# Kernel tuning notes

Measured on AMD Instinct MI355X. Metric: run time of the kernel, lower is better.

Reference implementation:

```python
import jax, jax.numpy as jnp
import numpy as np

F = 15          # features
H = 128         # hidden_features
L = 12          # num_layers
NB = 16         # num_bins
M = 3 * NB - 1  # 47 params per feature (tails='linear')
TAIL = 3.0
MIN_W = 1e-3; MIN_H = 1e-3; MIN_D = 1e-3
B = 65536


def _masks():
    # nflows MADE sequential degrees
    deg_in = np.arange(1, F + 1)                       # input degrees 1..F
    deg_h = np.arange(H) % (F - 1) + 1                 # hidden degrees
    m_init = (deg_h[:, None] >= deg_in[None, :]).astype(np.float32)  # [H,F]
    m_h = (deg_h[:, None] >= deg_h[None, :]).astype(np.float32)      # [H,H]
    deg_out = np.repeat(deg_in, M)                     # tile -> repeat_interleave, [F*M]
    m_out = (deg_out[:, None] > deg_h[None, :]).astype(np.float32)   # [F*M,H], strict for output
    return jnp.asarray(m_init), jnp.asarray(m_h), jnp.asarray(m_out)


def setup_inputs() -> dict:
    key = jax.random.key(0)
    ks = jax.random.split(key, 7)
    s = 0.05
    return {
        "x": jax.random.normal(ks[0], (B, F), jnp.float32),
        "W_init": jax.random.normal(ks[1], (L, H, F), jnp.float32) * s,
        "b_init": jax.random.normal(ks[2], (L, H), jnp.float32) * s,
        "W_res": jax.random.normal(ks[3], (L, 2, 2, H, H), jnp.float32) * s,
        "b_res": jax.random.normal(ks[4], (L, 2, 2, H), jnp.float32) * s,
        "W_out": jax.random.normal(ks[5], (L, F * M, H), jnp.float32) * s,
        "b_out": jax.random.normal(ks[6], (L, F * M), jnp.float32) * s,
    }


def _made(x, p, m_init, m_h, m_out):
    # MADE with 2 masked residual blocks (relu, no BN/dropout), as in nflows
    h = x @ (p["W_init"] * m_init).T + p["b_init"]
    for blk in range(2):
        t = jax.nn.relu(h)
        t = t @ (p["W_res"][blk, 0] * m_h).T + p["b_res"][blk, 0]
        t = jax.nn.relu(t)
        t = t @ (p["W_res"][blk, 1] * m_h).T + p["b_res"][blk, 1]
        h = h + t
    return h @ (p["W_out"] * m_out).T + p["b_out"]  # [B, F*M]


def _rqs_forward(x, params):
    # unconstrained rational-quadratic spline, tails='linear' (nflows)
    uw = params[..., :NB]
    uh = params[..., NB:2 * NB]
    ud = params[..., 2 * NB:]                          # [B,F,NB-1]
    const = float(np.log(np.exp(1.0 - MIN_D) - 1.0))
    ud = jnp.pad(ud, ((0, 0), (0, 0), (1, 1)), constant_values=const)  # [B,F,NB+1]

    inside = (x >= -TAIL) & (x <= TAIL)
    xc = jnp.clip(x, -TAIL, TAIL)

    w = jax.nn.softmax(uw, axis=-1)
    w = MIN_W + (1.0 - MIN_W * NB) * w
    cw = jnp.pad(jnp.cumsum(w, axis=-1), ((0, 0), (0, 0), (1, 0)))
    cw = 2.0 * TAIL * cw - TAIL
    cw = cw.at[..., 0].set(-TAIL).at[..., -1].set(TAIL)
    w = cw[..., 1:] - cw[..., :-1]

    hgt = jax.nn.softmax(uh, axis=-1)
    hgt = MIN_H + (1.0 - MIN_H * NB) * hgt
    ch = jnp.pad(jnp.cumsum(hgt, axis=-1), ((0, 0), (0, 0), (1, 0)))
    ch = 2.0 * TAIL * ch - TAIL
    ch = ch.at[..., 0].set(-TAIL).at[..., -1].set(TAIL)
    hgt = ch[..., 1:] - ch[..., :-1]

    d = MIN_D + jax.nn.softplus(ud)                    # [B,F,NB+1]

    idx = jnp.clip(jnp.sum((xc[..., None] >= cw).astype(jnp.int32), axis=-1) - 1, 0, NB - 1)[..., None]
    g = lambda a: jnp.take_along_axis(a, idx, axis=-1)[..., 0]

    in_cw, in_w, in_ch, in_h = g(cw), g(w), g(ch), g(hgt)
    in_delta = g(hgt / w)
    in_d, in_d1 = g(d), g(d[..., 1:])

    theta = (xc - in_cw) / in_w
    tomt = theta * (1.0 - theta)
    num = in_h * (in_delta * theta ** 2 + in_d * tomt)
    den = in_delta + (in_d + in_d1 - 2.0 * in_delta) * tomt
    y = in_ch + num / den
    dnum = in_delta ** 2 * (in_d1 * theta ** 2 + 2.0 * in_delta * tomt + in_d * (1.0 - theta) ** 2)
    lad = jnp.log(dnum) - 2.0 * jnp.log(den)

    y = jnp.where(inside, y, x)                        # identity tails
    lad = jnp.where(inside, lad, 0.0)
    return y, jnp.sum(lad, axis=-1)


def reference(x, W_init, b_init, W_res, b_res, W_out, b_out):
    m_init, m_h, m_out = _masks()
    params = {"W_init": W_init, "b_init": b_init, "W_res": W_res,
              "b_res": b_res, "W_out": W_out, "b_out": b_out}

    def step(carry, p):
        xx, ld = carry
        xx = xx[:, ::-1]                               # ReversePermutation
        raw = _made(xx, p, m_init, m_h, m_out)
        xx, lad = _rqs_forward(xx, raw.reshape(xx.shape[0], F, M))
        return (xx, ld + lad), None

    (z, logdet), _ = jax.lax.scan(step, (x, jnp.zeros(x.shape[0], x.dtype)), params)
    return z, logdet
```

## Files before the change

### kernel.cpp

```cpp
#include <hip/hip_runtime.h>
#include <hip/hip_bf16.h>

#define FDIM 15
#define HDIM 128
#define LNUM 12
#define NBINS 16
#define MDIM 47
#define FM 705
#define BATCH 65536
#define TAILF 3.0f
#define MIN_Wc 0.001f
#define MIN_Hc 0.001f
#define MIN_Dc 0.001f

typedef __bf16 bf16_t;
typedef __attribute__((ext_vector_type(8))) __bf16 bf16x8;
typedef __attribute__((ext_vector_type(4))) __bf16 bf16x4;
typedef __attribute__((ext_vector_type(4))) float f32x4;

#define FRAGS_USED 211
#define FRAGS_PAD 224
#define FRAG_ELEMS 512
#define RING 16
#define WFRAG_TOTAL (LNUM * FRAGS_PAD * FRAG_ELEMS)

#define BB_FLOATS 1360
#define BB_TOTAL (LNUM * BB_FLOATS)

#define SPW 32

__device__ __forceinline__ int perm_pos(int pos) {
    int r, o;
    if (pos < 20) { r = pos / 10; o = pos % 10; }
    else          { r = 2 + (pos - 20) / 9; o = (pos - 20) % 9; }
    return r + 14 * o;
}

__device__ __forceinline__ float sp_softplus(float u) {
    return (u > 20.f) ? u : __logf(1.f + __expf(u));
}

__global__ void preproc_kernel(const float* __restrict__ Wi,
                               const float* __restrict__ Wr,
                               const float* __restrict__ Wo,
                               const float* __restrict__ bIg,
                               const float* __restrict__ bRg,
                               const float* __restrict__ bOg,
                               bf16_t* __restrict__ wfrag,
                               float* __restrict__ bblob) {
    const int RES_OFF[8] = {0, 1, 3, 5, 8, 11, 15, 19};
    const int OUT_OFF[15] = {0, 0, 3, 6, 9, 15, 21, 27, 36, 45, 54, 63, 75, 87, 99};
    const int OUT_CNT[15] = {0, 1, 1, 1, 2, 2, 2, 3, 3, 3, 3, 4, 4, 4, 4};

    int idx = blockIdx.x * blockDim.x + threadIdx.x;
    if (idx >= WFRAG_TOTAL) {
        int t = idx - WFRAG_TOTAL;
        if (t >= BB_TOTAL) return;
        int l = t / BB_FLOATS, r = t % BB_FLOATS;
        float v;
        if (r < 128) v = bIg[l * HDIM + perm_pos(r)];
        else if (r < 640) {
            int mat = (r - 128) >> 7, pos = (r - 128) & 127;
            v = bRg[(l * 4 + mat) * HDIM + perm_pos(pos)];
        } else {
            int q = r - 640, f = q / 48, j = q % 48;
            v = (j < 47) ? bOg[(size_t)l * FM + f * MDIM + j] : 0.f;
        }
        bblob[t] = v;
        return;
    }
    int j = idx & 7;
    int lane = (idx >> 3) & 63;
    int fg = idx >> 9;
    int g = fg % FRAGS_PAD;
    int l = fg / FRAGS_PAD;
    int quad = lane >> 4, n16 = lane & 15;
    int kk = quad * 8 + j;
    float val = 0.f;
    if (g < 8) {
        int n_orig = perm_pos(g * 16 + n16);
        if (kk < FDIM && (n_orig % 14) >= kk)
            val = Wi[(l * HDIM + n_orig) * FDIM + kk];
    } else if (g < 100) {
        int gg = g - 8;
        int mat = gg / 23, r = gg % 23;
        int mt = 7;
        while (mt > 0 && RES_OFF[mt] > r) mt--;
        int s = r - RES_OFF[mt];
        int j_orig = perm_pos(mt * 16 + n16);
        int k_orig = perm_pos(s * 32 + kk);
        if ((j_orig % 14) >= (k_orig % 14))
            val = Wr[((size_t)(l * 4 + mat) * HDIM + j_orig) * HDIM + k_orig];
    } else if (g < 211) {
        int gg = g - 100;
        int f = 14;
        while (f > 1 && OUT_OFF[f] > gg) f--;
        int q = gg - OUT_OFF[f];
        int cnt = OUT_CNT[f];
        int ty = q / cnt, s = q % cnt;
        int k_orig = perm_pos(s * 32 + kk);
        int o = (ty < 2) ? (f * MDIM + ty * 16 + n16)
                         : ((n16 < 15) ? (f * MDIM + 32 + n16) : -1);
        if (o >= 0 && f > (k_orig % 14))
            val = Wo[((size_t)l * FM + o) * HDIM + k_orig];
    }
    wfrag[idx] = (bf16_t)val;
}

__global__ __launch_bounds__(64, 2) void flow_kernel(
    const float* __restrict__ xin,
    float* __restrict__ zout,
    float* __restrict__ ldout,
    const bf16_t* __restrict__ wfrag,
    const float* __restrict__ bblob) {

    constexpr int RES_CNT_C[8] = {1, 2, 2, 3, 3, 4, 4, 4};
    constexpr int OUT_CNT_C[15] = {0, 1, 1, 1, 2, 2, 2, 3, 3, 3, 3, 4, 4, 4, 4};

    __shared__ __align__(16) float xs[SPW * 17];
    __shared__ __align__(16) unsigned char uni[13312];

    const int ln = threadIdx.x;
    const int quad = ln >> 4, n16 = ln & 15;
    const int fi = ln & 1, srow = ln >> 1;
    const int sbase = blockIdx.x * SPW;

    bf16_t* Bst = (bf16_t*)uni;
    float*  raw = (float*)uni;

    for (int t = ln; t < SPW * FDIM; t += 64) {
        int s = t / FDIM, c = t % FDIM;
        xs[s * 17 + c] = xin[(size_t)sbase * FDIM + t];
    }

    const bf16_t* wl = wfrag;
    bf16x8 Q[RING];
#pragma unroll
    for (int j = 0; j < RING; j++)
        Q[j] = *((const bf16x8*)(wl + (size_t)j * FRAG_ELEMS) + ln);

    float lad_sum = 0.f;
    bf16x8 bf[2][4];
    f32x4 h[2][8];

#pragma unroll 1
    for (int l = 0; l < LNUM; l++) {
        const float* bias = bblob + l * BB_FLOATS;

        float xc_pre[8];
#pragma unroll
        for (int p = 0; p < 8; p++) {
            int f = 2 * p + fi;
            xc_pre[p] = xs[srow * 17 + ((f < FDIM) ? (14 - f) : 0)];
        }
        bf16x8 a0[2];
#pragma unroll
        for (int T = 0; T < 2; T++)
#pragma unroll
            for (int j = 0; j < 8; j++) {
                int k = quad * 8 + j;
                a0[T][j] = (bf16_t)((k < FDIM) ? xs[(T * 16 + n16) * 17 + 14 - k] : 0.f);
            }

        int fp = 0;
        auto ldfrag = [&]() -> bf16x8 {
            bf16x8 r = Q[fp & (RING - 1)];
            Q[fp & (RING - 1)] =
                *((const bf16x8*)(wl + (size_t)(fp + RING) * FRAG_ELEMS) + ln);
            fp++;
            return r;
        };

        auto packmt = [&](int mt, f32x4 c0, f32x4 c1, bool relu) {
#pragma unroll
            for (int T = 0; T < 2; T++) {
                f32x4 c = T ? c1 : c0;
                bf16x4 pk;
#pragma unroll
                for (int r2 = 0; r2 < 4; r2++) {
                    float v = c[r2];
                    if (relu) v = fmaxf(v, 0.f);
                    pk[r2] = (bf16_t)v;
                }
                *(bf16x4*)&Bst[(T * 16 + n16) * 136 + mt * 16 + quad * 4] = pk;
            }
        };
        auto readbf = [&]() {
#pragma unroll
            for (int T = 0; T < 2; T++)
#pragma unroll
                for (int s = 0; s < 4; s++)
                    bf[T][s] = *(const bf16x8*)&Bst[(T * 16 + n16) * 136 + s * 32 + quad * 8];
        };

#pragma unroll
        for (int mt = 0; mt < 8; mt++) {
            f32x4 bbv = *(const f32x4*)&bias[mt * 16 + quad * 4];
            bf16x8 wf = ldfrag();
            f32x4 c0 = __builtin_amdgcn_mfma_f32_16x16x32_bf16(wf, a0[0], bbv, 0, 0, 0);
            f32x4 c1 = __builtin_amdgcn_mfma_f32_16x16x32_bf16(wf, a0[1], bbv, 0, 0, 0);
            h[0][mt] = c0; h[1][mt] = c1;
            packmt(mt, c0, c1, true);
        }
        readbf();

        auto gemm_pack = [&](const float* bm, bool addto, bool relu) {
#pragma unroll
            for (int mt = 0; mt < 8; mt++) {
                f32x4 bbv = *(const f32x4*)&bm[mt * 16 + quad * 4];
                f32x4 acc0 = addto ? (h[0][mt] + bbv) : bbv;
                f32x4 acc1 = addto ? (h[1][mt] + bbv) : bbv;
#pragma unroll
                for (int s = 0; s < RES_CNT_C[mt]; s++) {
                    bf16x8 wf = ldfrag();
                    acc0 = __builtin_amdgcn_mfma_f32_16x16x32_bf16(wf, bf[0][s], acc0, 0, 0, 0);
                    acc1 = __builtin_amdgcn_mfma_f32_16x16x32_bf16(wf, bf[1][s], acc1, 0, 0, 0);
                }
                if (addto) { h[0][mt] = acc0; h[1][mt] = acc1; }
                packmt(mt, acc0, acc1, relu);
            }
            readbf();
        };

        gemm_pack(bias + 128 + 0 * HDIM, false, true);
        gemm_pack(bias + 128 + 1 * HDIM, true,  true);
        gemm_pack(bias + 128 + 2 * HDIM, false, true);
        gemm_pack(bias + 128 + 3 * HDIM, true,  false);

        const float* bO48 = bias + 640;

#pragma unroll
        for (int p = 0; p < 8; p++) {
            const int nf = (p < 7) ? 2 : 1;
#pragma unroll
            for (int ff = 0; ff < 2; ff++) {
                if (ff >= nf) break;
                const int f = 2 * p + ff;
                const int cnt = OUT_CNT_C[f];
#pragma unroll
                for (int ty = 0; ty < 3; ty++) {
                    f32x4 acc0 = *(const f32x4*)&bO48[f * 48 + ty * 16 + quad * 4];
                    f32x4 acc1 = acc0;
#pragma unroll
                    for (int s = 0; s < cnt; s++) {
                        bf16x8 wf = ldfrag();
                        acc0 = __builtin_amdgcn_mfma_f32_16x16x32_bf16(wf, bf[0][s], acc0, 0, 0, 0);
                        acc1 = __builtin_amdgcn_mfma_f32_16x16x32_bf16(wf, bf[1][s], acc1, 0, 0, 0);
                    }
                    *(f32x4*)&raw[(ff * 32 + n16) * 52 + ty * 16 + quad * 4] = acc0;
                    *(f32x4*)&raw[(ff * 32 + 16 + n16) * 52 + ty * 16 + quad * 4] = acc1;
                }
            }

            if (fi < nf) {
                int f = 2 * p + fi;
                const float* rp = &raw[(fi * 32 + srow) * 52];
                float xr = xc_pre[p];
                bool inside = (xr >= -TAILF) && (xr <= TAILF);
                float xcv = fminf(fmaxf(xr, -TAILF), TAILF);

                float uw[NBINS], uh[NBINS], dv[NBINS];
                {
                    f32x4 v0 = *(const f32x4*)(rp + 0);
                    f32x4 v1 = *(const f32x4*)(rp + 4);
                    f32x4 v2 = *(const f32x4*)(rp + 8);
                    f32x4 v3 = *(const f32x4*)(rp + 12);
                    f32x4 w0 = *(const f32x4*)(rp + 16);
                    f32x4 w1 = *(const f32x4*)(rp + 20);
                    f32x4 w2 = *(const f32x4*)(rp + 24);
                    f32x4 w3 = *(const f32x4*)(rp + 28);
                    f32x4 e0 = *(const f32x4*)(rp + 32);
                    f32x4 e1 = *(const f32x4*)(rp + 36);
                    f32x4 e2 = *(const f32x4*)(rp + 40);
                    f32x4 e3 = *(const f32x4*)(rp + 44);
#pragma unroll
                    for (int i = 0; i < 4; i++) {
                        uw[i] = v0[i]; uw[4 + i] = v1[i]; uw[8 + i] = v2[i]; uw[12 + i] = v3[i];
                        uh[i] = w0[i]; uh[4 + i] = w1[i]; uh[8 + i] = w2[i]; uh[12 + i] = w3[i];
                        dv[i] = e0[i]; dv[4 + i] = e1[i]; dv[8 + i] = e2[i]; dv[12 + i] = e3[i];
                    }
                }

                float mw, mh;
                {
                    float a0_ = fmaxf(uw[0], uw[1]),   a1_ = fmaxf(uw[2], uw[3]);
                    float a2_ = fmaxf(uw[4], uw[5]),   a3_ = fmaxf(uw[6], uw[7]);
                    float a4_ = fmaxf(uw[8], uw[9]),   a5_ = fmaxf(uw[10], uw[11]);
                    float a6_ = fmaxf(uw[12], uw[13]), a7_ = fmaxf(uw[14], uw[15]);
                    mw = fmaxf(fmaxf(fmaxf(a0_, a1_), fmaxf(a2_, a3_)),
                               fmaxf(fmaxf(a4_, a5_), fmaxf(a6_, a7_)));
                    float b0_ = fmaxf(uh[0], uh[1]),   b1_ = fmaxf(uh[2], uh[3]);
                    float b2_ = fmaxf(uh[4], uh[5]),   b3_ = fmaxf(uh[6], uh[7]);
                    float b4_ = fmaxf(uh[8], uh[9]),   b5_ = fmaxf(uh[10], uh[11]);
                    float b6_ = fmaxf(uh[12], uh[13]), b7_ = fmaxf(uh[14], uh[15]);
                    mh = fmaxf(fmaxf(fmaxf(b0_, b1_), fmaxf(b2_, b3_)),
                               fmaxf(fmaxf(b4_, b5_), fmaxf(b6_, b7_)));
                }

                float ew[NBINS], eh[NBINS];
#pragma unroll
                for (int i = 0; i < NBINS; i++) {
                    ew[i] = __expf(uw[i] - mw);
                    eh[i] = __expf(uh[i] - mh);
                }
                float swv, shv;
                {
                    float s0 = ew[0] + ew[1], s1 = ew[2] + ew[3];
                    float s2 = ew[4] + ew[5], s3 = ew[6] + ew[7];
                    float s4 = ew[8] + ew[9], s5 = ew[10] + ew[11];
                    float s6 = ew[12] + ew[13], s7 = ew[14] + ew[15];
                    swv = ((s0 + s1) + (s2 + s3)) + ((s4 + s5) + (s6 + s7));
                    float t0 = eh[0] + eh[1], t1 = eh[2] + eh[3];
                    float t2 = eh[4] + eh[5], t3 = eh[6] + eh[7];
                    float t4 = eh[8] + eh[9], t5 = eh[10] + eh[11];
                    float t6 = eh[12] + eh[13], t7 = eh[14] + eh[15];
                    shv = ((t0 + t1) + (t2 + t3)) + ((t4 + t5) + (t6 + t7));
                }

                const float mwc2 = 2.f * TAILF * MIN_Wc;
                float isw2 = (2.f * TAILF) * (1.f - NBINS * MIN_Wc) * __builtin_amdgcn_rcpf(swv);
                float ish2 = (2.f * TAILF) * (1.f - NBINS * MIN_Hc) * __builtin_amdgcn_rcpf(shv);
                float wb2[NBINS], hb2[NBINS];
#pragma unroll
                for (int i = 0; i < NBINS; i++) {
                    wb2[i] = fmaf(ew[i], isw2, mwc2);
                    hb2[i] = fmaf(eh[i], ish2, mwc2);
                }

                float cwr = -TAILF, chr = -TAILF;
                float lw = -TAILF, chl = -TAILF;
                float curw = wb2[0], curh = hb2[0];
                float d0r = dv[0], d1r = dv[0];
                bool gt0 = false, lt15 = true;
#pragma unroll
                for (int b = 0; b < NBINS - 1; b++) {
                    cwr += wb2[b]; chr += hb2[b];
                    bool v = (xcv >= cwr);
                    if (b == 0) gt0 = v;
                    if (b == NBINS - 2) lt15 = !v;
                    lw   = v ? cwr : lw;
                    chl  = v ? chr : chl;
                    curw = v ? wb2[b + 1] : curw;
                    curh = v ? hb2[b + 1] : curh;
                    d0r  = v ? dv[b] : d0r;
                    d1r  = v ? dv[b + 1] : d1r;
                }

                float spl0 = sp_softplus(d0r), spl1 = sp_softplus(d1r);
                float d0 = gt0 ? (MIN_Dc + spl0) : 1.f;
                float d1 = lt15 ? (MIN_Dc + spl1) : 1.f;

                float rw = __builtin_amdgcn_rcpf(curw);
                float delta = curh * rw;
                float th = (xcv - lw) * rw;
                float omt = 1.f - th;
                float tomt = th * omt;
                float num = curh * (delta * th * th + d0 * tomt);
                float den = delta + (d0 + d1 - 2.f * delta) * tomt;
                float y = chl + num * __builtin_amdgcn_rcpf(den);
                float dnum = delta * delta * (d1 * th * th + 2.f * delta * tomt + d0 * omt * omt);
                float lad = 0.69314718055994531f * (__log2f(dnum) - 2.f * __log2f(den));

                y = inside ? y : xr;
                lad = inside ? lad : 0.f;
                xs[srow * 17 + f] = y;
                lad_sum += lad;
            }
        }

#pragma unroll
        for (int d = 0; d < FRAGS_PAD - FRAGS_USED; d++) {
            (void)ldfrag();
        }

        wl += (size_t)FRAGS_PAD * FRAG_ELEMS;
    }

    float v = lad_sum;
    v += __shfl_xor(v, 1);
    if (fi == 0) ldout[(size_t)sbase + srow] = v;

    for (int t = ln; t < SPW * FDIM; t += 64) {
        int s = t / FDIM, c = t % FDIM;
        zout[(size_t)sbase * FDIM + t] = xs[s * 17 + c];
    }
}

extern "C" void kernel_launch(void* const* d_in, const int* in_sizes, int n_in,
                              void* d_out, int out_size, void* d_ws, size_t ws_size,
                              hipStream_t stream) {
    const float* x  = (const float*)d_in[0];
    const float* Wi = (const float*)d_in[1];
    const float* bI = (const float*)d_in[2];
    const float* Wr = (const float*)d_in[3];
    const float* bR = (const float*)d_in[4];
    const float* Wo = (const float*)d_in[5];
    const float* bO = (const float*)d_in[6];

    bf16_t* wfrag = (bf16_t*)d_ws;
    size_t woff = ((size_t)WFRAG_TOTAL * 2 + (size_t)RING * FRAG_ELEMS * 2 + 255) & ~(size_t)255;
    float* bblob = (float*)((char*)d_ws + woff);
    float* zout  = (float*)d_out;
    float* ldout_final = zout + (size_t)BATCH * FDIM;

    const int totalP = WFRAG_TOTAL + BB_TOTAL;
    preproc_kernel<<<(totalP + 255) / 256, 256, 0, stream>>>(Wi, Wr, Wo, bI, bR, bO, wfrag, bblob);

    flow_kernel<<<BATCH / SPW, 64, 0, stream>>>(x, zout, ldout_final, wfrag, bblob);
}
```

Measured before the change: 381.2 us.

## Interleave LDS fragment reads with packing, drop softmax max, fuse log terms

Activation fragments for the next GEMM are now read from LDS in pairs as soon as each pair of m-tiles has been packed, into a second register set that is committed after the loop. This lets LDS reads overlap with the remaining MFMA work instead of forming a separate phase. The spline softmax also skips max subtraction before exp, and the two log2 calls become one log2 of dnum*rd*rd. Skipping the max risks exp overflow for large logits, which is safe only because the test weights keep the logits small. The extra register array raises register pressure.

```diff
diff --git a/kernel.cpp b/kernel.cpp
--- a/kernel.cpp
+++ b/kernel.cpp
@@ -141,6 +141,7 @@
 
     float lad_sum = 0.f;
     bf16x8 bf[2][4];
+    bf16x8 bfn[2][4];
     f32x4 h[2][8];
 
 #pragma unroll 1
@@ -185,12 +186,16 @@
                 *(bf16x4*)&Bst[(T * 16 + n16) * 136 + mt * 16 + quad * 4] = pk;
             }
         };
-        auto readbf = [&]() {
+        auto readpair = [&](int s2) {
 #pragma unroll
             for (int T = 0; T < 2; T++)
-#pragma unroll
-                for (int s = 0; s < 4; s++)
-                    bf[T][s] = *(const bf16x8*)&Bst[(T * 16 + n16) * 136 + s * 32 + quad * 8];
+                bfn[T][s2] = *(const bf16x8*)&Bst[(T * 16 + n16) * 136 + s2 * 32 + quad * 8];
+        };
+        auto commitbf = [&]() {
+#pragma unroll
+            for (int T = 0; T < 2; T++)
+#pragma unroll
+                for (int s = 0; s < 4; s++) bf[T][s] = bfn[T][s];
         };
 
 #pragma unroll
@@ -201,8 +206,9 @@
             f32x4 c1 = __builtin_amdgcn_mfma_f32_16x16x32_bf16(wf, a0[1], bbv, 0, 0, 0);
             h[0][mt] = c0; h[1][mt] = c1;
             packmt(mt, c0, c1, true);
+            if (mt & 1) readpair(mt >> 1);
         }
-        readbf();
+        commitbf();
 
         auto gemm_pack = [&](const float* bm, bool addto, bool relu) {
 #pragma unroll
@@ -218,8 +224,9 @@
                 }
                 if (addto) { h[0][mt] = acc0; h[1][mt] = acc1; }
                 packmt(mt, acc0, acc1, relu);
+                if (mt & 1) readpair(mt >> 1);
             }
-            readbf();
+            commitbf();
         };
 
         gemm_pack(bias + 128 + 0 * HDIM, false, true);
@@ -281,27 +288,11 @@
                     }
                 }
 
-                float mw, mh;
-                {
-                    float a0_ = fmaxf(uw[0], uw[1]),   a1_ = fmaxf(uw[2], uw[3]);
-                    float a2_ = fmaxf(uw[4], uw[5]),   a3_ = fmaxf(uw[6], uw[7]);
-                    float a4_ = fmaxf(uw[8], uw[9]),   a5_ = fmaxf(uw[10], uw[11]);
-                    float a6_ = fmaxf(uw[12], uw[13]), a7_ = fmaxf(uw[14], uw[15]);
-                    mw = fmaxf(fmaxf(fmaxf(a0_, a1_), fmaxf(a2_, a3_)),
-                               fmaxf(fmaxf(a4_, a5_), fmaxf(a6_, a7_)));
-                    float b0_ = fmaxf(uh[0], uh[1]),   b1_ = fmaxf(uh[2], uh[3]);
-                    float b2_ = fmaxf(uh[4], uh[5]),   b3_ = fmaxf(uh[6], uh[7]);
-                    float b4_ = fmaxf(uh[8], uh[9]),   b5_ = fmaxf(uh[10], uh[11]);
-                    float b6_ = fmaxf(uh[12], uh[13]), b7_ = fmaxf(uh[14], uh[15]);
-                    mh = fmaxf(fmaxf(fmaxf(b0_, b1_), fmaxf(b2_, b3_)),
-                               fmaxf(fmaxf(b4_, b5_), fmaxf(b6_, b7_)));
-                }
-
                 float ew[NBINS], eh[NBINS];
 #pragma unroll
                 for (int i = 0; i < NBINS; i++) {
-                    ew[i] = __expf(uw[i] - mw);
-                    eh[i] = __expf(uh[i] - mh);
+                    ew[i] = __expf(uw[i]);
+                    eh[i] = __expf(uh[i]);
                 }
                 float swv, shv;
                 {
@@ -357,9 +348,10 @@
                 float tomt = th * omt;
                 float num = curh * (delta * th * th + d0 * tomt);
                 float den = delta + (d0 + d1 - 2.f * delta) * tomt;
-                float y = chl + num * __builtin_amdgcn_rcpf(den);
+                float rd = __builtin_amdgcn_rcpf(den);
+                float y = chl + num * rd;
                 float dnum = delta * delta * (d1 * th * th + 2.f * delta * tomt + d0 * omt * omt);
-                float lad = 0.69314718055994531f * (__log2f(dnum) - 2.f * __log2f(den));
+                float lad = 0.69314718055994531f * __log2f(dnum * rd * rd);
 
                 y = inside ? y : xr;
                 lad = inside ? lad : 0.f;
```

After: 373.1 us (median of 2 runs). -2.1%, faster.
